# Kernel tuning notes

Measured on AMD Instinct MI355X. Metric: run time of the kernel, lower is better.

Reference implementation:

```python
import jax, jax.numpy as jnp
import numpy as np
from jax import lax

B, C, H, W = 2, 64, 128, 128
F_SCALE, STRIDE = 2, 2
F = F_SCALE * STRIDE            # pixel-unshuffle factor = 4
CK = C // 16                    # attention channel dim = 4
SCALE_DIM = C // F_SCALE        # softmax scale uses embed_size//f_scale = 32


def setup_inputs() -> dict:
    key = jax.random.key(0)
    ks = jax.random.split(key, 16)
    g = lambda i, shape, s=0.05: jax.random.normal(ks[i], shape, jnp.float32) * s
    return {
        "x":   jax.random.normal(ks[0], (B, C, H, W), jnp.float32),
        # conv1 = Sequential(1x1 C->CK, 1x1 CK->CK)
        "w1a": g(1, (CK, C)), "b1a": g(2, (CK,)),
        "w1b": g(3, (CK, CK)), "b1b": g(4, (CK,)),
        # wqk parameter (torch.randn, std 1)
        "wqk": jax.random.normal(ks[5], (CK, CK), jnp.float32),
        # conv2: 1x1 CK->C ; conv: 1x1 C->C
        "w2":  g(6, (C, CK)), "b2": g(7, (C,)),
        "wc":  g(8, (C, C)), "bc": g(9, (C,)),
        # FF (GridSANaive): 1x1 C->C/4, 3x3 dilated C/4->C/4, 1x1 C/4->C
        "wf1": g(10, (C // 4, C)), "bf1": g(11, (C // 4,)),
        "wf2": g(12, (C // 4, C // 4, 3, 3)), "bf2": g(13, (C // 4,)),
        "wf3": g(14, (C, C // 4)), "bf3": g(15, (C,)),
    }


def conv1x1(x, w, b):
    return jnp.einsum('bchw,oc->bohw', x, w) + b[None, :, None, None]


def grid_attention(x, wqk):
    b, c, h, w = x.shape
    sh = h // 2
    x = jnp.pad(x, ((0, 0), (0, 0), (sh, 0), (0, 0)))      # Shift2d pad (top)
    # F.layer_norm over last 3 dims, no affine, eps=1e-5
    mu = jnp.mean(x, axis=(1, 2, 3), keepdims=True)
    var = jnp.var(x, axis=(1, 2, 3), keepdims=True)
    xx = (x - mu) / jnp.sqrt(var + 1e-5)
    hh, ww = xx.shape[2], xx.shape[3]
    ph, pw = (F - hh % F) % F, (F - ww % F) % F
    xx = jnp.pad(xx, ((0, 0), (0, 0), (0, ph), (0, pw)))
    gh, gw = (hh + ph) // F, (ww + pw) // F
    # pixel_unshuffle: channel layout (c, fy, fx)
    xx = xx.reshape(b, c, gh, F, gw, F).transpose(0, 1, 3, 5, 2, 4)
    xx = xx.reshape(b, c * F * F, gh, gw)
    # rearrange 'b (f c) h w -> (b f) c h w', f=F*F (mixes layout, as in original)
    xx = xx.reshape(b * F * F, c, gh, gw)
    L = gh * gw
    tok = xx.transpose(0, 2, 3, 1).reshape(b * F * F, L, c)   # (bg, L, c)
    qk = tok @ wqk
    qk = qk / (jnp.linalg.norm(qk, axis=-1, keepdims=True) + 1e-8)
    attn = (jnp.einsum('blk,bmk->blm', qk, qk) + 1.0) / (SCALE_DIM ** 0.5)
    attn = jax.nn.softmax(attn, axis=-1)
    out = jnp.einsum('blm,bmc->blc', attn, tok)
    out = out.reshape(b * F * F, gh, gw, c).transpose(0, 3, 1, 2)
    out = out.reshape(b, F * F * c, gh, gw)
    # pixel_shuffle: channel layout (fy, fx, c)
    out = out.reshape(b, F, F, c, gh, gw).transpose(0, 3, 4, 1, 5, 2)
    out = out.reshape(b, c, gh * F, gw * F)
    out = out[:, :, :hh, :ww]                               # undo shuffle pad
    return out[:, :, :-sh, :] if sh > 0 else out            # Shift2d crop (bottom)


def ff(x, wf1, bf1, wf2, bf2, wf3, bf3):
    h1 = jax.nn.relu(conv1x1(x, wf1, bf1))
    k = 1 + (STRIDE // 2) * 2   # ShiftConv2d offset for 3x3, dilation=STRIDE
    hp = jnp.pad(h1, ((0, 0), (0, 0), (k, 0), (0, 0)))
    h2 = lax.conv_general_dilated(
        hp, wf2, (1, 1), ((STRIDE, STRIDE), (STRIDE, STRIDE)),
        rhs_dilation=(STRIDE, STRIDE),
        dimension_numbers=('NCHW', 'OIHW', 'NCHW'))
    h2 = jax.nn.relu((h2 + bf2[None, :, None, None])[:, :, :-k, :])
    return conv1x1(h2, wf3, bf3)


def reference(x, w1a, b1a, w1b, b1b, wqk, w2, b2, wc, bc,
              wf1, bf1, wf2, bf2, wf3, bf3):
    a = conv1x1(conv1x1(x, w1a, b1a), w1b, b1b)
    att = grid_attention(a, wqk)
    y = x + conv1x1(conv1x1(att, w2, b2), wc, bc)
    return y + ff(y, wf1, bf1, wf2, bf2, wf3, bf3)
```

## Files before the change

### kernel.cpp

```cpp
#include <hip/hip_runtime.h>
#include <math.h>

#define CHW  (64*16384)
#define ATT_SCALE 0.17677669529663687f

__global__ __launch_bounds__(256) void k1_a_stats(
    const float* __restrict__ x, const float* __restrict__ w1a,
    const float* __restrict__ b1a, const float* __restrict__ w1b,
    const float* __restrict__ b1b, float* __restrict__ a,
    float* __restrict__ statsbuf) {
  __shared__ float sA[256];
  __shared__ float sb1[4];
  __shared__ float pc[4][4][256];
  __shared__ float rs[64], rq[64];
  int tid = threadIdx.x;
  {
    int o = tid >> 6, c = tid & 63;
    float s = 0.f;
    #pragma unroll
    for (int k = 0; k < 4; ++k) s += w1b[o*4+k] * w1a[k*64+c];
    sA[tid] = s;
  }
  if (tid < 4) {
    float s = b1b[tid];
    #pragma unroll
    for (int k = 0; k < 4; ++k) s += w1b[tid*4+k] * b1a[k];
    sb1[tid] = s;
  }
  __syncthreads();
  int quad = tid & 15, cg = tid >> 4;
  int gq = blockIdx.x * 16 + quad;
  int bb = gq >> 12;
  int px0 = (gq & 4095) * 4;
  const float* xp = x + bb*CHW + (cg*4)*16384 + px0;
  float4 acc[4];
  #pragma unroll
  for (int o = 0; o < 4; ++o) acc[o] = make_float4(0.f,0.f,0.f,0.f);
  #pragma unroll
  for (int cc = 0; cc < 4; ++cc) {
    float4 xv = *(const float4*)(xp + cc*16384);
    int c = cg*4 + cc;
    #pragma unroll
    for (int o = 0; o < 4; ++o) {
      float w = sA[o*64+c];
      acc[o].x += w*xv.x; acc[o].y += w*xv.y; acc[o].z += w*xv.z; acc[o].w += w*xv.w;
    }
  }
  #pragma unroll
  for (int o = 0; o < 4; ++o) {
    pc[0][o][tid] = acc[o].x; pc[1][o][tid] = acc[o].y;
    pc[2][o][tid] = acc[o].z; pc[3][o][tid] = acc[o].w;
  }
  __syncthreads();
  if (tid < 64) {
    int q2 = tid & 15, o = tid >> 4;
    float sx=0.f, sy=0.f, sz=0.f, sw=0.f;
    #pragma unroll
    for (int g2 = 0; g2 < 16; ++g2) {
      int idx = g2*16 + q2;
      sx += pc[0][o][idx]; sy += pc[1][o][idx];
      sz += pc[2][o][idx]; sw += pc[3][o][idx];
    }
    float bv = sb1[o];
    sx += bv; sy += bv; sz += bv; sw += bv;
    int gq2 = blockIdx.x*16 + q2;
    int b2 = gq2 >> 12; int p0 = (gq2 & 4095)*4;
    *(float4*)(a + b2*4*16384 + o*16384 + p0) = make_float4(sx,sy,sz,sw);
    rs[tid] = sx+sy+sz+sw;
    rq[tid] = sx*sx+sy*sy+sz*sz+sw*sw;
  }
  __syncthreads();
  for (int s2 = 32; s2; s2 >>= 1) {
    if (tid < s2) { rs[tid] += rs[tid+s2]; rq[tid] += rq[tid+s2]; }
    __syncthreads();
  }
  if (tid == 0) { statsbuf[blockIdx.x*2] = rs[0]; statsbuf[blockIdx.x*2+1] = rq[0]; }
}

__global__ __launch_bounds__(256) void k2_tok_qk(
    const float* __restrict__ a, const float* __restrict__ statsbuf,
    const float* __restrict__ wqk, float4* __restrict__ tok,
    float4* __restrict__ qko) {
  __shared__ float rs[256], rq[256];
  int tid = threadIdx.x;
  int g = blockIdx.x / 6;
  int t = (blockIdx.x % 6) * 256 + tid;
  int b = g >> 4, u = (g >> 2) & 3, v = g & 3;
  rs[tid] = statsbuf[(b*256+tid)*2];
  rq[tid] = statsbuf[(b*256+tid)*2+1];
  __syncthreads();
  for (int s2 = 128; s2; s2 >>= 1) {
    if (tid < s2) { rs[tid] += rs[tid+s2]; rq[tid] += rq[tid+s2]; }
    __syncthreads();
  }
  float mu  = rs[0] * (1.f/98304.f);
  float var = rq[0] * (1.f/98304.f) - mu*mu;
  float rsig = rsqrtf(var + 1e-5f);
  int i = t >> 5, j = t & 31;
  int Hp = i*4 + v;
  float4 tv;
  if (Hp >= 64) {
    tv = *(const float4*)(a + (b*4+u)*16384 + (Hp-64)*128 + j*4);
    tv.x = (tv.x-mu)*rsig; tv.y = (tv.y-mu)*rsig;
    tv.z = (tv.z-mu)*rsig; tv.w = (tv.w-mu)*rsig;
  } else {
    float z = -mu*rsig;
    tv = make_float4(z,z,z,z);
  }
  float q0 = tv.x*wqk[0] + tv.y*wqk[4] + tv.z*wqk[8]  + tv.w*wqk[12];
  float q1 = tv.x*wqk[1] + tv.y*wqk[5] + tv.z*wqk[9]  + tv.w*wqk[13];
  float q2 = tv.x*wqk[2] + tv.y*wqk[6] + tv.z*wqk[10] + tv.w*wqk[14];
  float q3 = tv.x*wqk[3] + tv.y*wqk[7] + tv.z*wqk[11] + tv.w*wqk[15];
  float nrm = sqrtf(q0*q0 + q1*q1 + q2*q2 + q3*q3);
  float inv = 1.f / (nrm + 1e-8f);
  int idx = g*1536 + t;
  tok[idx] = tv;
  qko[idx] = make_float4(q0*inv, q1*inv, q2*inv, q3*inv);
}

__device__ __forceinline__ float poly_exp(float d) {
  return 1.f + d*(1.f + d*(0.5f + d*(0.16666667f + d*0.04166667f)));
}
__global__ __launch_bounds__(512) void k3_attn(
    const float4* __restrict__ tok, const float4* __restrict__ qk,
    float* __restrict__ att) {
  __shared__ float4 kq[1024];
  __shared__ float4 kt[1024];
  __shared__ float red[16][5][128];
  int tid = threadIdx.x;
  int g = blockIdx.x >> 3, qb = blockIdx.x & 7;
  const float4* qg = qk  + g*1536;
  const float4* tg = tok + g*1536;
  for (int m = tid; m < 1024; m += 512) { kq[m] = qg[512+m]; kt[m] = tg[512+m]; }
  __syncthreads();
  int qi = tid & 31, s = tid >> 5;
  int t0 = qb*128 + qi*4;
  float4 q[4];
  #pragma unroll
  for (int j = 0; j < 4; ++j) {
    float4 v = qg[t0+j];
    q[j] = make_float4(v.x*ATT_SCALE, v.y*ATT_SCALE, v.z*ATT_SCALE, v.w*ATT_SCALE);
  }
  float den[4] = {0.f,0.f,0.f,0.f};
  float4 ov[4];
  #pragma unroll
  for (int j = 0; j < 4; ++j) ov[j] = make_float4(0.f,0.f,0.f,0.f);
  if (s == 0) {
    float4 k0 = qg[0]; float4 tv0 = tg[0];
    #pragma unroll
    for (int j = 0; j < 4; ++j) {
      float d = q[j].x*k0.x + q[j].y*k0.y + q[j].z*k0.z + q[j].w*k0.w;
      float e = 512.f * poly_exp(d);
      den[j] += e;
      ov[j].x += e*tv0.x; ov[j].y += e*tv0.y; ov[j].z += e*tv0.z; ov[j].w += e*tv0.w;
    }
  }
  int m0 = s * 64;
  #pragma unroll 2
  for (int m = m0; m < m0 + 64; ++m) {
    float4 kk = kq[m];
    float4 tv = kt[m];
    #pragma unroll
    for (int j = 0; j < 4; ++j) {
      float d = q[j].x*kk.x + q[j].y*kk.y + q[j].z*kk.z + q[j].w*kk.w;
      float e = poly_exp(d);
      den[j] += e;
      ov[j].x += e*tv.x; ov[j].y += e*tv.y; ov[j].z += e*tv.z; ov[j].w += e*tv.w;
    }
  }
  #pragma unroll
  for (int j = 0; j < 4; ++j) {
    int key = j*32 + qi;
    red[s][0][key] = den[j];
    red[s][1][key] = ov[j].x; red[s][2][key] = ov[j].y;
    red[s][3][key] = ov[j].z; red[s][4][key] = ov[j].w;
  }
  __syncthreads();
  if (tid < 128) {
    int qi_r = tid & 31, j_r = tid >> 5;
    float dsum=0.f, ox=0.f, oy=0.f, oz=0.f, ow=0.f;
    #pragma unroll
    for (int ss = 0; ss < 16; ++ss) {
      dsum += red[ss][0][tid];
      ox += red[ss][1][tid]; oy += red[ss][2][tid];
      oz += red[ss][3][tid]; ow += red[ss][4][tid];
    }
    float inv = 1.f / dsum;
    int t = qb*128 + qi_r*4 + j_r;
    int b = g >> 4, u = (g >> 2) & 3, v = g & 3;
    int i = t >> 5, j = t & 31;
    float* ap = att + b*4*16384 + (i*4+u)*128 + (j*4+v);
    ap[0]     = ox*inv;
    ap[16384] = oy*inv;
    ap[32768] = oz*inv;
    ap[49152] = ow*inv;
  }
}

__global__ __launch_bounds__(512) void k4_y_h1(
    const float* __restrict__ x, const float* __restrict__ att,
    const float* __restrict__ w2p, const float* __restrict__ b2p,
    const float* __restrict__ wcp, const float* __restrict__ bcp,
    const float* __restrict__ wf1, const float* __restrict__ bf1,
    float* __restrict__ yout, float* __restrict__ h1) {
  __shared__ float sWf[64][4];
  __shared__ float sbf[64];
  __shared__ float sw1[1024];
  __shared__ float sb1[16];
  __shared__ float4 satt[4][32];
  __shared__ float4 ylds[64][32];
  int tid = threadIdx.x;
  if (tid < 256) {
    int o = tid >> 2, k = tid & 3;
    float s = 0.f;
    for (int c = 0; c < 64; ++c) s += wcp[o*64+c] * w2p[c*4+k];
    sWf[o][k] = s;
  }
  if (tid < 64) {
    float s = bcp[tid];
    for (int c = 0; c < 64; ++c) s += wcp[tid*64+c] * b2p[c];
    sbf[tid] = s;
  }
  for (int i = tid; i < 1024; i += 512) sw1[i] = wf1[i];
  if (tid < 16) sb1[tid] = bf1[tid];
  int quad = tid & 31, og = tid >> 5;
  int gq = blockIdx.x*32 + quad;
  int bb = gq >> 12; int px0 = (gq & 4095)*4;
  if (tid < 128) {
    int k = tid >> 5, q2 = tid & 31;
    int gq2 = blockIdx.x*32 + q2;
    int b2i = gq2 >> 12; int p0 = (gq2 & 4095)*4;
    satt[k][q2] = *(const float4*)(att + b2i*4*16384 + k*16384 + p0);
  }
  __syncthreads();
  float4 a0 = satt[0][quad], a1 = satt[1][quad], a2 = satt[2][quad], a3 = satt[3][quad];
  const float* xp = x + bb*CHW + px0;
  float* yp = yout + bb*CHW + px0;
  #pragma unroll
  for (int cc = 0; cc < 4; ++cc) {
    int c = og*4 + cc;
    float4 xv = *(const float4*)(xp + c*16384);
    float w0 = sWf[c][0], w1 = sWf[c][1], w2v = sWf[c][2], w3 = sWf[c][3];
    float bv = sbf[c];
    float4 yv;
    yv.x = xv.x + w0*a0.x + w1*a1.x + w2v*a2.x + w3*a3.x + bv;
    yv.y = xv.y + w0*a0.y + w1*a1.y + w2v*a2.y + w3*a3.y + bv;
    yv.z = xv.z + w0*a0.z + w1*a1.z + w2v*a2.z + w3*a3.z + bv;
    yv.w = xv.w + w0*a0.w + w1*a1.w + w2v*a2.w + w3*a3.w + bv;
    *(float4*)(yp + c*16384) = yv;
    ylds[c][quad] = yv;
  }
  __syncthreads();
  float bv = sb1[og];
  float4 acc = make_float4(bv, bv, bv, bv);
  #pragma unroll 8
  for (int c = 0; c < 64; ++c) {
    float4 yv = ylds[c][quad];
    float wa = sw1[og*64+c];
    acc.x += wa*yv.x; acc.y += wa*yv.y; acc.z += wa*yv.z; acc.w += wa*yv.w;
  }
  acc.x = fmaxf(acc.x,0.f); acc.y = fmaxf(acc.y,0.f);
  acc.z = fmaxf(acc.z,0.f); acc.w = fmaxf(acc.w,0.f);
  *(float4*)(h1 + bb*16*16384 + og*16384 + px0) = acc;
}

__global__ __launch_bounds__(512) void k6_ff_out(
    const float* __restrict__ h1, const float* __restrict__ wf2,
    const float* __restrict__ bf2, const float* __restrict__ wf3,
    const float* __restrict__ bf3, float* yo) {
  __shared__ float sbuf[16][3][136];
  __shared__ float h2buf[128][21];
  int tid = threadIdx.x;
  int bb = blockIdx.x >> 7, h = blockIdx.x & 127;
  for (int idx = tid; idx < 16*3*136; idx += 512) {
    int c = idx / (3*136);
    int r = (idx / 136) % 3;
    int col = idx % 136;
    int row = h - 5 + 2*r;
    int w = col - 4;
    float v = 0.f;
    if (row >= 0 && w >= 0 && w < 128)
      v = h1[bb*16*16384 + c*16384 + row*128 + w];
    sbuf[c][r][col] = v;
  }
  __syncthreads();
  int w = tid & 127;
  int g = __builtin_amdgcn_readfirstlane(tid >> 7);
  float acc[4];
  #pragma unroll
  for (int o = 0; o < 4; ++o) acc[o] = bf2[g*4+o];
  #pragma unroll 4
  for (int c = 0; c < 16; ++c) {
    #pragma unroll
    for (int r = 0; r < 3; ++r) {
      float tm2 = sbuf[c][r][w+2];
      float t00 = sbuf[c][r][w+4];
      float tp2 = sbuf[c][r][w+6];
      #pragma unroll
      for (int o = 0; o < 4; ++o) {
        const float* wp = wf2 + (((g*4+o)*16 + c)*3 + r)*3;
        acc[o] += wp[0]*tm2 + wp[1]*t00 + wp[2]*tp2;
      }
    }
  }
  #pragma unroll
  for (int o = 0; o < 4; ++o) h2buf[w][g*4+o] = fmaxf(acc[o], 0.f);
  __syncthreads();
  float hv[16];
  #pragma unroll
  for (int k = 0; k < 16; ++k) hv[k] = h2buf[w][k];
  float* ybase = yo + bb*CHW + h*128 + w;
  #pragma unroll 4
  for (int oc = 0; oc < 16; ++oc) {
    int o = g*16 + oc;
    float sv = bf3[o] + ybase[o*16384];
    #pragma unroll
    for (int k = 0; k < 16; ++k) sv += wf3[o*16+k]*hv[k];
    ybase[o*16384] = sv;
  }
}

extern "C" void kernel_launch(void* const* d_in, const int* in_sizes, int n_in,
                              void* d_out, int out_size, void* d_ws, size_t ws_size,
                              hipStream_t stream) {
  (void)in_sizes; (void)n_in; (void)out_size; (void)ws_size;
  const float* x   = (const float*)d_in[0];
  const float* w1a = (const float*)d_in[1];
  const float* b1a = (const float*)d_in[2];
  const float* w1b = (const float*)d_in[3];
  const float* b1b = (const float*)d_in[4];
  const float* wqk = (const float*)d_in[5];
  const float* w2  = (const float*)d_in[6];
  const float* b2  = (const float*)d_in[7];
  const float* wc  = (const float*)d_in[8];
  const float* bc  = (const float*)d_in[9];
  const float* wf1 = (const float*)d_in[10];
  const float* bf1 = (const float*)d_in[11];
  const float* wf2 = (const float*)d_in[12];
  const float* bf2 = (const float*)d_in[13];
  const float* wf3 = (const float*)d_in[14];
  const float* bf3 = (const float*)d_in[15];

  float* ws = (float*)d_ws;
  float*  a_    = ws;
  float*  stats = ws + 131072;
  float4* tok   = (float4*)(ws + 132096);
  float4* qkb   = (float4*)(ws + 328704);
  float*  att   = ws + 525312;
  float*  h1    = ws + 656384;
  float*  y     = (float*)d_out;

  k1_a_stats<<<512, 256, 0, stream>>>(x, w1a, b1a, w1b, b1b, a_, stats);
  k2_tok_qk <<<192, 256, 0, stream>>>(a_, stats, wqk, tok, qkb);
  k3_attn   <<<256, 512, 0, stream>>>(tok, qkb, att);
  k4_y_h1   <<<256, 512, 0, stream>>>(x, att, w2, b2, wc, bc, wf1, bf1, y, h1);
  k6_ff_out <<<256, 512, 0, stream>>>(h1, wf2, bf2, wf3, bf3, y);
}
```

Measured before the change: 134.1 us.

## Fuse token/QK prep into attention and fuse y, FF stages into one kernel

Merges the normalization and QK projection kernel into the attention kernel, so each block builds the key/value tokens in shared memory straight from the conv output. Because the padded tokens are all identical, they are computed analytically and only the real rows are attended as queries. The y residual, FF conv1, dilated 3x3 conv and final projection now run in one per-row kernel that recomputes h1 for the three needed rows, which removes the y and h1 round trips through global memory and two launches. In exchange the x reads and h1 work are recomputed redundantly about three times.

```diff
diff --git a/kernel.cpp b/kernel.cpp
--- a/kernel.cpp
+++ b/kernel.cpp
@@ -3,6 +3,10 @@
 
 #define CHW  (64*16384)
 #define ATT_SCALE 0.17677669529663687f
+
+__device__ __forceinline__ float poly_exp(float d) {
+  return 1.f + d*(1.f + d*(0.5f + d*(0.16666667f + d*0.04166667f)));
+}
 
 __global__ __launch_bounds__(256) void k1_a_stats(
     const float* __restrict__ x, const float* __restrict__ w1a,
@@ -77,82 +81,76 @@
   if (tid == 0) { statsbuf[blockIdx.x*2] = rs[0]; statsbuf[blockIdx.x*2+1] = rq[0]; }
 }
 
-__global__ __launch_bounds__(256) void k2_tok_qk(
+__global__ __launch_bounds__(512) void k23_attn(
     const float* __restrict__ a, const float* __restrict__ statsbuf,
-    const float* __restrict__ wqk, float4* __restrict__ tok,
-    float4* __restrict__ qko) {
-  __shared__ float rs[256], rq[256];
+    const float* __restrict__ wqk, float* __restrict__ att) {
+  __shared__ float4 kq[1024];
+  __shared__ float4 kt[1024];
+  __shared__ float red[8][5][64];
+  __shared__ float padr[8][5];
+  __shared__ float swqk[16];
+  __shared__ float padout[4];
   int tid = threadIdx.x;
-  int g = blockIdx.x / 6;
-  int t = (blockIdx.x % 6) * 256 + tid;
-  int b = g >> 4, u = (g >> 2) & 3, v = g & 3;
-  rs[tid] = statsbuf[(b*256+tid)*2];
-  rq[tid] = statsbuf[(b*256+tid)*2+1];
-  __syncthreads();
-  for (int s2 = 128; s2; s2 >>= 1) {
+  float* rs = &red[0][0][0];
+  float* rq = rs + 512;
+  rs[tid] = statsbuf[2*tid];
+  rq[tid] = statsbuf[2*tid+1];
+  if (tid < 16) swqk[tid] = wqk[tid];
+  __syncthreads();
+  for (int s2 = 256; s2; s2 >>= 1) {
     if (tid < s2) { rs[tid] += rs[tid+s2]; rq[tid] += rq[tid+s2]; }
     __syncthreads();
   }
   float mu  = rs[0] * (1.f/98304.f);
   float var = rq[0] * (1.f/98304.f) - mu*mu;
   float rsig = rsqrtf(var + 1e-5f);
-  int i = t >> 5, j = t & 31;
-  int Hp = i*4 + v;
-  float4 tv;
-  if (Hp >= 64) {
-    tv = *(const float4*)(a + (b*4+u)*16384 + (Hp-64)*128 + j*4);
+  int g = blockIdx.x >> 3, qb = blockIdx.x & 7;
+  int b = g >> 4, u = (g >> 2) & 3, v = g & 3;
+  const float* abase = a + ((b*4+u) << 14);
+  __syncthreads();
+  for (int km = tid; km < 1024; km += 512) {
+    int tt = 512 + km;
+    int i = tt >> 5, j = tt & 31;
+    int row = (i - 16)*4 + v;
+    float4 tv = *(const float4*)(abase + row*128 + (j << 2));
     tv.x = (tv.x-mu)*rsig; tv.y = (tv.y-mu)*rsig;
     tv.z = (tv.z-mu)*rsig; tv.w = (tv.w-mu)*rsig;
-  } else {
-    float z = -mu*rsig;
-    tv = make_float4(z,z,z,z);
-  }
-  float q0 = tv.x*wqk[0] + tv.y*wqk[4] + tv.z*wqk[8]  + tv.w*wqk[12];
-  float q1 = tv.x*wqk[1] + tv.y*wqk[5] + tv.z*wqk[9]  + tv.w*wqk[13];
-  float q2 = tv.x*wqk[2] + tv.y*wqk[6] + tv.z*wqk[10] + tv.w*wqk[14];
-  float q3 = tv.x*wqk[3] + tv.y*wqk[7] + tv.z*wqk[11] + tv.w*wqk[15];
-  float nrm = sqrtf(q0*q0 + q1*q1 + q2*q2 + q3*q3);
-  float inv = 1.f / (nrm + 1e-8f);
-  int idx = g*1536 + t;
-  tok[idx] = tv;
-  qko[idx] = make_float4(q0*inv, q1*inv, q2*inv, q3*inv);
-}
-
-__device__ __forceinline__ float poly_exp(float d) {
-  return 1.f + d*(1.f + d*(0.5f + d*(0.16666667f + d*0.04166667f)));
-}
-__global__ __launch_bounds__(512) void k3_attn(
-    const float4* __restrict__ tok, const float4* __restrict__ qk,
-    float* __restrict__ att) {
-  __shared__ float4 kq[1024];
-  __shared__ float4 kt[1024];
-  __shared__ float red[16][5][128];
-  int tid = threadIdx.x;
-  int g = blockIdx.x >> 3, qb = blockIdx.x & 7;
-  const float4* qg = qk  + g*1536;
-  const float4* tg = tok + g*1536;
-  for (int m = tid; m < 1024; m += 512) { kq[m] = qg[512+m]; kt[m] = tg[512+m]; }
-  __syncthreads();
-  int qi = tid & 31, s = tid >> 5;
-  int t0 = qb*128 + qi*4;
-  float4 q[4];
-  #pragma unroll
-  for (int j = 0; j < 4; ++j) {
-    float4 v = qg[t0+j];
-    q[j] = make_float4(v.x*ATT_SCALE, v.y*ATT_SCALE, v.z*ATT_SCALE, v.w*ATT_SCALE);
-  }
-  float den[4] = {0.f,0.f,0.f,0.f};
-  float4 ov[4];
-  #pragma unroll
-  for (int j = 0; j < 4; ++j) ov[j] = make_float4(0.f,0.f,0.f,0.f);
+    float q0 = tv.x*swqk[0] + tv.y*swqk[4] + tv.z*swqk[8]  + tv.w*swqk[12];
+    float q1 = tv.x*swqk[1] + tv.y*swqk[5] + tv.z*swqk[9]  + tv.w*swqk[13];
+    float q2 = tv.x*swqk[2] + tv.y*swqk[6] + tv.z*swqk[10] + tv.w*swqk[14];
+    float q3 = tv.x*swqk[3] + tv.y*swqk[7] + tv.z*swqk[11] + tv.w*swqk[15];
+    float nrm = sqrtf(q0*q0 + q1*q1 + q2*q2 + q3*q3);
+    float inv = 1.f / (nrm + 1e-8f);
+    kt[km] = tv;
+    kq[km] = make_float4(q0*inv, q1*inv, q2*inv, q3*inv);
+  }
+  float tpad = -mu * rsig;
+  float c0 = swqk[0]+swqk[4]+swqk[8]+swqk[12];
+  float c1 = swqk[1]+swqk[5]+swqk[9]+swqk[13];
+  float c2 = swqk[2]+swqk[6]+swqk[10]+swqk[14];
+  float c3 = swqk[3]+swqk[7]+swqk[11]+swqk[15];
+  float p0 = tpad*c0, p1 = tpad*c1, p2 = tpad*c2, p3 = tpad*c3;
+  float pn = sqrtf(p0*p0+p1*p1+p2*p2+p3*p3);
+  float pinv = 1.f / (pn + 1e-8f);
+  float4 qpu = make_float4(p0*pinv, p1*pinv, p2*pinv, p3*pinv);
+  __syncthreads();
+  int s = tid >> 5, qi = tid & 31;
+  float4 q[2];
+  #pragma unroll
+  for (int j = 0; j < 2; ++j) {
+    float4 vq = kq[qb*64 + j*32 + qi];
+    q[j] = make_float4(vq.x*ATT_SCALE, vq.y*ATT_SCALE, vq.z*ATT_SCALE, vq.w*ATT_SCALE);
+  }
+  float den[2] = {0.f, 0.f};
+  float4 ov[2];
+  ov[0] = make_float4(0.f,0.f,0.f,0.f); ov[1] = make_float4(0.f,0.f,0.f,0.f);
   if (s == 0) {
-    float4 k0 = qg[0]; float4 tv0 = tg[0];
-    #pragma unroll
-    for (int j = 0; j < 4; ++j) {
-      float d = q[j].x*k0.x + q[j].y*k0.y + q[j].z*k0.z + q[j].w*k0.w;
+    #pragma unroll
+    for (int j = 0; j < 2; ++j) {
+      float d = q[j].x*qpu.x + q[j].y*qpu.y + q[j].z*qpu.z + q[j].w*qpu.w;
       float e = 512.f * poly_exp(d);
       den[j] += e;
-      ov[j].x += e*tv0.x; ov[j].y += e*tv0.y; ov[j].z += e*tv0.z; ov[j].w += e*tv0.w;
+      ov[j].x += e*tpad; ov[j].y += e*tpad; ov[j].z += e*tpad; ov[j].w += e*tpad;
     }
   }
   int m0 = s * 64;
@@ -161,7 +159,7 @@
     float4 kk = kq[m];
     float4 tv = kt[m];
     #pragma unroll
-    for (int j = 0; j < 4; ++j) {
+    for (int j = 0; j < 2; ++j) {
       float d = q[j].x*kk.x + q[j].y*kk.y + q[j].z*kk.z + q[j].w*kk.w;
       float e = poly_exp(d);
       den[j] += e;
@@ -169,154 +167,228 @@
     }
   }
   #pragma unroll
-  for (int j = 0; j < 4; ++j) {
-    int key = j*32 + qi;
-    red[s][0][key] = den[j];
-    red[s][1][key] = ov[j].x; red[s][2][key] = ov[j].y;
-    red[s][3][key] = ov[j].z; red[s][4][key] = ov[j].w;
-  }
-  __syncthreads();
-  if (tid < 128) {
-    int qi_r = tid & 31, j_r = tid >> 5;
+  for (int j = 0; j < 2; ++j) {
+    den[j]  += __shfl_xor(den[j], 32);
+    ov[j].x += __shfl_xor(ov[j].x, 32);
+    ov[j].y += __shfl_xor(ov[j].y, 32);
+    ov[j].z += __shfl_xor(ov[j].z, 32);
+    ov[j].w += __shfl_xor(ov[j].w, 32);
+  }
+  if ((tid & 32) == 0) {
+    int hs = s >> 1;
+    #pragma unroll
+    for (int j = 0; j < 2; ++j) {
+      int slot = j*32 + qi;
+      red[hs][0][slot] = den[j];
+      red[hs][1][slot] = ov[j].x; red[hs][2][slot] = ov[j].y;
+      red[hs][3][slot] = ov[j].z; red[hs][4][slot] = ov[j].w;
+    }
+  }
+  {
+    float4 qs = make_float4(qpu.x*ATT_SCALE, qpu.y*ATT_SCALE, qpu.z*ATT_SCALE, qpu.w*ATT_SCALE);
+    float pd = 0.f, px = 0.f, py = 0.f, pz = 0.f, pw = 0.f;
+    #pragma unroll
+    for (int mm = 0; mm < 2; ++mm) {
+      int m = tid + mm*512;
+      float4 kk = kq[m]; float4 tv = kt[m];
+      float d = qs.x*kk.x + qs.y*kk.y + qs.z*kk.z + qs.w*kk.w;
+      float e = poly_exp(d);
+      pd += e; px += e*tv.x; py += e*tv.y; pz += e*tv.z; pw += e*tv.w;
+    }
+    if (tid == 0) {
+      float d = qs.x*qpu.x + qs.y*qpu.y + qs.z*qpu.z + qs.w*qpu.w;
+      float e = 512.f * poly_exp(d);
+      pd += e; px += e*tpad; py += e*tpad; pz += e*tpad; pw += e*tpad;
+    }
+    #pragma unroll
+    for (int mask = 1; mask < 64; mask <<= 1) {
+      pd += __shfl_xor(pd, mask);
+      px += __shfl_xor(px, mask); py += __shfl_xor(py, mask);
+      pz += __shfl_xor(pz, mask); pw += __shfl_xor(pw, mask);
+    }
+    if ((tid & 63) == 0) {
+      int wv = tid >> 6;
+      padr[wv][0] = pd; padr[wv][1] = px; padr[wv][2] = py;
+      padr[wv][3] = pz; padr[wv][4] = pw;
+    }
+  }
+  __syncthreads();
+  if (tid < 64) {
     float dsum=0.f, ox=0.f, oy=0.f, oz=0.f, ow=0.f;
     #pragma unroll
-    for (int ss = 0; ss < 16; ++ss) {
+    for (int ss = 0; ss < 8; ++ss) {
       dsum += red[ss][0][tid];
       ox += red[ss][1][tid]; oy += red[ss][2][tid];
       oz += red[ss][3][tid]; ow += red[ss][4][tid];
     }
     float inv = 1.f / dsum;
-    int t = qb*128 + qi_r*4 + j_r;
-    int b = g >> 4, u = (g >> 2) & 3, v = g & 3;
+    int t = 512 + qb*64 + tid;
     int i = t >> 5, j = t & 31;
-    float* ap = att + b*4*16384 + (i*4+u)*128 + (j*4+v);
+    float* ap = att + b*65536 + (i*4+u)*128 + (j*4+v);
     ap[0]     = ox*inv;
     ap[16384] = oy*inv;
     ap[32768] = oz*inv;
     ap[49152] = ow*inv;
+  } else if (tid == 64) {
+    float dsum=0.f, ox=0.f, oy=0.f, oz=0.f, ow=0.f;
+    #pragma unroll
+    for (int wv = 0; wv < 8; ++wv) {
+      dsum += padr[wv][0];
+      ox += padr[wv][1]; oy += padr[wv][2]; oz += padr[wv][3]; ow += padr[wv][4];
+    }
+    float inv = 1.f / dsum;
+    padout[0] = ox*inv; padout[1] = oy*inv; padout[2] = oz*inv; padout[3] = ow*inv;
+  }
+  __syncthreads();
+  if (qb == 0) {
+    int i = tid >> 5, j = tid & 31;
+    float* ap = att + b*65536 + (i*4+u)*128 + (j*4+v);
+    ap[0] = padout[0]; ap[16384] = padout[1];
+    ap[32768] = padout[2]; ap[49152] = padout[3];
   }
 }
 
-__global__ __launch_bounds__(512) void k4_y_h1(
+__global__ __launch_bounds__(512) void k46_out(
     const float* __restrict__ x, const float* __restrict__ att,
     const float* __restrict__ w2p, const float* __restrict__ b2p,
     const float* __restrict__ wcp, const float* __restrict__ bcp,
     const float* __restrict__ wf1, const float* __restrict__ bf1,
-    float* __restrict__ yout, float* __restrict__ h1) {
-  __shared__ float sWf[64][4];
-  __shared__ float sbf[64];
-  __shared__ float sw1[1024];
+    const float* __restrict__ wf2, const float* __restrict__ bf2,
+    const float* __restrict__ wf3, const float* __restrict__ bf3,
+    float* __restrict__ out) {
+  __shared__ float4 sWf4[64];
+  __shared__ float sbfc[64];
+  __shared__ __align__(16) float sw1t[64*16];
   __shared__ float sb1[16];
-  __shared__ float4 satt[4][32];
-  __shared__ float4 ylds[64][32];
+  __shared__ __align__(16) float sW2t[144*16];
+  __shared__ float sb2[16];
+  __shared__ __align__(16) float sw3[1024];
+  __shared__ float sb3[64];
+  __shared__ float satt[4][4][128];
+  __shared__ float sh1[16][3][132];
+  __shared__ float sh2[128][17];
   int tid = threadIdx.x;
+  int bb = blockIdx.x >> 7, h = blockIdx.x & 127;
   if (tid < 256) {
     int o = tid >> 2, k = tid & 3;
     float s = 0.f;
     for (int c = 0; c < 64; ++c) s += wcp[o*64+c] * w2p[c*4+k];
-    sWf[o][k] = s;
-  }
-  if (tid < 64) {
-    float s = bcp[tid];
-    for (int c = 0; c < 64; ++c) s += wcp[tid*64+c] * b2p[c];
-    sbf[tid] = s;
-  }
-  for (int i = tid; i < 1024; i += 512) sw1[i] = wf1[i];
+    ((float*)&sWf4[o])[k] = s;
+  } else if (tid < 320) {
+    int o = tid - 256;
+    float s = bcp[o];
+    for (int c = 0; c < 64; ++c) s += wcp[o*64+c] * b2p[c];
+    sbfc[o] = s;
+  }
+  for (int i2 = tid; i2 < 1024; i2 += 512) {
+    int c = i2 >> 4, o2 = i2 & 15;
+    sw1t[i2] = wf1[o2*64 + c];
+  }
+  for (int i2 = tid; i2 < 2304; i2 += 512) {
+    int o2 = i2 & 15, rest = i2 >> 4;
+    int t = rest % 3, r = (rest/3) % 3, c = rest/9;
+    sW2t[i2] = wf2[((o2*16 + c)*3 + r)*3 + t];
+  }
+  for (int i2 = tid; i2 < 1024; i2 += 512) sw3[i2] = wf3[i2];
   if (tid < 16) sb1[tid] = bf1[tid];
-  int quad = tid & 31, og = tid >> 5;
-  int gq = blockIdx.x*32 + quad;
-  int bb = gq >> 12; int px0 = (gq & 4095)*4;
-  if (tid < 128) {
-    int k = tid >> 5, q2 = tid & 31;
-    int gq2 = blockIdx.x*32 + q2;
-    int b2i = gq2 >> 12; int p0 = (gq2 & 4095)*4;
-    satt[k][q2] = *(const float4*)(att + b2i*4*16384 + k*16384 + p0);
-  }
-  __syncthreads();
-  float4 a0 = satt[0][quad], a1 = satt[1][quad], a2 = satt[2][quad], a3 = satt[3][quad];
-  const float* xp = x + bb*CHW + px0;
-  float* yp = yout + bb*CHW + px0;
-  #pragma unroll
-  for (int cc = 0; cc < 4; ++cc) {
-    int c = og*4 + cc;
-    float4 xv = *(const float4*)(xp + c*16384);
-    float w0 = sWf[c][0], w1 = sWf[c][1], w2v = sWf[c][2], w3 = sWf[c][3];
-    float bv = sbf[c];
-    float4 yv;
-    yv.x = xv.x + w0*a0.x + w1*a1.x + w2v*a2.x + w3*a3.x + bv;
-    yv.y = xv.y + w0*a0.y + w1*a1.y + w2v*a2.y + w3*a3.y + bv;
-    yv.z = xv.z + w0*a0.z + w1*a1.z + w2v*a2.z + w3*a3.z + bv;
-    yv.w = xv.w + w0*a0.w + w1*a1.w + w2v*a2.w + w3*a3.w + bv;
-    *(float4*)(yp + c*16384) = yv;
-    ylds[c][quad] = yv;
-  }
-  __syncthreads();
-  float bv = sb1[og];
-  float4 acc = make_float4(bv, bv, bv, bv);
-  #pragma unroll 8
+  else if (tid < 32) sb2[tid-16] = bf2[tid-16];
+  else if (tid < 96) sb3[tid-32] = bf3[tid-32];
+  {
+    int k = tid >> 7, w = tid & 127;
+    int rows[4] = {h-5, h-3, h-1, h};
+    #pragma unroll
+    for (int rr = 0; rr < 4; ++rr) {
+      int row = rows[rr];
+      satt[rr][k][w] = (row >= 0) ? att[bb*65536 + k*16384 + row*128 + w] : 0.f;
+    }
+  }
+  if (tid < 192) {
+    int c = tid / 12, rem = tid % 12;
+    int r = rem >> 2, cp = rem & 3;
+    int col = (cp < 2) ? cp : (130 + cp - 2);
+    sh1[c][r][col] = 0.f;
+  }
+  __syncthreads();
+  int w = tid & 127, og = tid >> 7;
+  float att4[3][4];
+  #pragma unroll
+  for (int rr = 0; rr < 3; ++rr)
+    #pragma unroll
+    for (int k = 0; k < 4; ++k) att4[rr][k] = satt[rr][k][w];
+  float acc[3][4];
+  #pragma unroll
+  for (int r = 0; r < 3; ++r)
+    #pragma unroll
+    for (int o = 0; o < 4; ++o) acc[r][o] = sb1[og*4+o];
+  int r0 = h-5, r1 = h-3, r2 = h-1;
+  bool ok0 = r0 >= 0, ok1 = r1 >= 0, ok2 = r2 >= 0;
+  const float* xb = x + bb*CHW + w;
   for (int c = 0; c < 64; ++c) {
-    float4 yv = ylds[c][quad];
-    float wa = sw1[og*64+c];
-    acc.x += wa*yv.x; acc.y += wa*yv.y; acc.z += wa*yv.z; acc.w += wa*yv.w;
-  }
-  acc.x = fmaxf(acc.x,0.f); acc.y = fmaxf(acc.y,0.f);
-  acc.z = fmaxf(acc.z,0.f); acc.w = fmaxf(acc.w,0.f);
-  *(float4*)(h1 + bb*16*16384 + og*16384 + px0) = acc;
-}
-
-__global__ __launch_bounds__(512) void k6_ff_out(
-    const float* __restrict__ h1, const float* __restrict__ wf2,
-    const float* __restrict__ bf2, const float* __restrict__ wf3,
-    const float* __restrict__ bf3, float* yo) {
-  __shared__ float sbuf[16][3][136];
-  __shared__ float h2buf[128][21];
-  int tid = threadIdx.x;
-  int bb = blockIdx.x >> 7, h = blockIdx.x & 127;
-  for (int idx = tid; idx < 16*3*136; idx += 512) {
-    int c = idx / (3*136);
-    int r = (idx / 136) % 3;
-    int col = idx % 136;
-    int row = h - 5 + 2*r;
-    int w = col - 4;
-    float v = 0.f;
-    if (row >= 0 && w >= 0 && w < 128)
-      v = h1[bb*16*16384 + c*16384 + row*128 + w];
-    sbuf[c][r][col] = v;
-  }
-  __syncthreads();
-  int w = tid & 127;
-  int g = __builtin_amdgcn_readfirstlane(tid >> 7);
-  float acc[4];
-  #pragma unroll
-  for (int o = 0; o < 4; ++o) acc[o] = bf2[g*4+o];
-  #pragma unroll 4
+    const float* xc = xb + c*16384;
+    float4 wf = sWf4[c];
+    float bv = sbfc[c];
+    float4 s1 = *(const float4*)&sw1t[c*16 + og*4];
+    if (ok0) {
+      float yv = xc[r0*128] + wf.x*att4[0][0] + wf.y*att4[0][1] + wf.z*att4[0][2] + wf.w*att4[0][3] + bv;
+      acc[0][0] += s1.x*yv; acc[0][1] += s1.y*yv; acc[0][2] += s1.z*yv; acc[0][3] += s1.w*yv;
+    }
+    if (ok1) {
+      float yv = xc[r1*128] + wf.x*att4[1][0] + wf.y*att4[1][1] + wf.z*att4[1][2] + wf.w*att4[1][3] + bv;
+      acc[1][0] += s1.x*yv; acc[1][1] += s1.y*yv; acc[1][2] += s1.z*yv; acc[1][3] += s1.w*yv;
+    }
+    if (ok2) {
+      float yv = xc[r2*128] + wf.x*att4[2][0] + wf.y*att4[2][1] + wf.z*att4[2][2] + wf.w*att4[2][3] + bv;
+      acc[2][0] += s1.x*yv; acc[2][1] += s1.y*yv; acc[2][2] += s1.z*yv; acc[2][3] += s1.w*yv;
+    }
+  }
+  #pragma unroll
+  for (int o = 0; o < 4; ++o) {
+    sh1[og*4+o][0][w+2] = ok0 ? fmaxf(acc[0][o], 0.f) : 0.f;
+    sh1[og*4+o][1][w+2] = ok1 ? fmaxf(acc[1][o], 0.f) : 0.f;
+    sh1[og*4+o][2][w+2] = ok2 ? fmaxf(acc[2][o], 0.f) : 0.f;
+  }
+  __syncthreads();
+  float h2[4];
+  #pragma unroll
+  for (int o = 0; o < 4; ++o) h2[o] = sb2[og*4+o];
   for (int c = 0; c < 16; ++c) {
     #pragma unroll
     for (int r = 0; r < 3; ++r) {
-      float tm2 = sbuf[c][r][w+2];
-      float t00 = sbuf[c][r][w+4];
-      float tp2 = sbuf[c][r][w+6];
-      #pragma unroll
-      for (int o = 0; o < 4; ++o) {
-        const float* wp = wf2 + (((g*4+o)*16 + c)*3 + r)*3;
-        acc[o] += wp[0]*tm2 + wp[1]*t00 + wp[2]*tp2;
-      }
-    }
-  }
-  #pragma unroll
-  for (int o = 0; o < 4; ++o) h2buf[w][g*4+o] = fmaxf(acc[o], 0.f);
+      float tm = sh1[c][r][w];
+      float t0 = sh1[c][r][w+2];
+      float tp = sh1[c][r][w+4];
+      int base = ((c*3 + r)*3) << 4;
+      float4 w0 = *(const float4*)&sW2t[base + og*4];
+      float4 w1 = *(const float4*)&sW2t[base + 16 + og*4];
+      float4 w2v = *(const float4*)&sW2t[base + 32 + og*4];
+      h2[0] += w0.x*tm + w1.x*t0 + w2v.x*tp;
+      h2[1] += w0.y*tm + w1.y*t0 + w2v.y*tp;
+      h2[2] += w0.z*tm + w1.z*t0 + w2v.z*tp;
+      h2[3] += w0.w*tm + w1.w*t0 + w2v.w*tp;
+    }
+  }
+  #pragma unroll
+  for (int o = 0; o < 4; ++o) sh2[w][og*4+o] = fmaxf(h2[o], 0.f);
   __syncthreads();
   float hv[16];
   #pragma unroll
-  for (int k = 0; k < 16; ++k) hv[k] = h2buf[w][k];
-  float* ybase = yo + bb*CHW + h*128 + w;
+  for (int k = 0; k < 16; ++k) hv[k] = sh2[w][k];
+  float a0h = satt[3][0][w], a1h = satt[3][1][w], a2h = satt[3][2][w], a3h = satt[3][3][w];
+  const float* xr = x + bb*CHW + h*128 + w;
+  float* orow = out + bb*CHW + h*128 + w;
   #pragma unroll 4
   for (int oc = 0; oc < 16; ++oc) {
-    int o = g*16 + oc;
-    float sv = bf3[o] + ybase[o*16384];
-    #pragma unroll
-    for (int k = 0; k < 16; ++k) sv += wf3[o*16+k]*hv[k];
-    ybase[o*16384] = sv;
+    int o = og*16 + oc;
+    float4 wf = sWf4[o];
+    float yv = xr[o*16384] + wf.x*a0h + wf.y*a1h + wf.z*a2h + wf.w*a3h + sbfc[o];
+    float sv = yv + sb3[o];
+    const float4* s3 = (const float4*)&sw3[o*16];
+    float4 s30 = s3[0], s31 = s3[1], s32 = s3[2], s33 = s3[3];
+    sv += s30.x*hv[0] + s30.y*hv[1] + s30.z*hv[2] + s30.w*hv[3];
+    sv += s31.x*hv[4] + s31.y*hv[5] + s31.z*hv[6] + s31.w*hv[7];
+    sv += s32.x*hv[8] + s32.y*hv[9] + s32.z*hv[10] + s32.w*hv[11];
+    sv += s33.x*hv[12] + s33.y*hv[13] + s33.z*hv[14] + s33.w*hv[15];
+    orow[o*16384] = sv;
   }
 }
 
@@ -342,17 +414,12 @@
   const float* bf3 = (const float*)d_in[15];
 
   float* ws = (float*)d_ws;
-  float*  a_    = ws;
-  float*  stats = ws + 131072;
-  float4* tok   = (float4*)(ws + 132096);
-  float4* qkb   = (float4*)(ws + 328704);
-  float*  att   = ws + 525312;
-  float*  h1    = ws + 656384;
-  float*  y     = (float*)d_out;
+  float* a_    = ws;
+  float* stats = ws + 131072;
+  float* att   = ws + 132096;
 
   k1_a_stats<<<512, 256, 0, stream>>>(x, w1a, b1a, w1b, b1b, a_, stats);
-  k2_tok_qk <<<192, 256, 0, stream>>>(a_, stats, wqk, tok, qkb);
-  k3_attn   <<<256, 512, 0, stream>>>(tok, qkb, att);
-  k4_y_h1   <<<256, 512, 0, stream>>>(x, att, w2, b2, wc, bc, wf1, bf1, y, h1);
-  k6_ff_out <<<256, 512, 0, stream>>>(h1, wf2, bf2, wf3, bf3, y);
+  k23_attn  <<<256, 512, 0, stream>>>(a_, stats, wqk, att);
+  k46_out   <<<256, 512, 0, stream>>>(x, att, w2, b2, wc, bc, wf1, bf1,
+                                      wf2, bf2, wf3, bf3, (float*)d_out);
 }
```

After: 175.6 us. 1.31x slower.
